# Kernel optimization log

Measured on AMD Instinct MI355X. Metric: run time of the kernel, lower is better.

The kernel has to match this reference:

```python
import jax, jax.numpy as jnp
import numpy as np
import math

D_MODEL = 1024
NUM_HEADS = 16
D_K = D_MODEL // NUM_HEADS
THETA = 10000.0
NEG_INF = 1.0e6  # module uses -1e6, not -inf


def _rope_tables(seq_len):
    pair_idx = jnp.arange(0, D_K, 2, dtype=jnp.float32)
    inv_freq = 1.0 / (THETA ** (pair_idx / D_K))
    pos = jnp.arange(seq_len, dtype=jnp.float32)
    angles = jnp.outer(pos, inv_freq)  # (S, D_K//2)
    return jnp.cos(angles), jnp.sin(angles)


def _apply_rope(x, cos, sin):
    # x: (B, H, S, D_K); cos/sin: (S, D_K//2)
    xe = x[..., 0::2]
    xo = x[..., 1::2]
    oe = xe * cos - xo * sin
    oo = xe * sin + xo * cos
    return jnp.stack([oe, oo], axis=-1).reshape(x.shape)


def setup_inputs() -> dict:
    key = jax.random.key(0)
    k0, k1, k2, k3, k4 = jax.random.split(key, 5)
    B, S = 2, 2048
    x = jax.random.normal(k0, (B, S, D_MODEL), dtype=jnp.float32)
    scale = 0.02
    wq = jax.random.normal(k1, (D_MODEL, D_MODEL), dtype=jnp.float32) * scale
    wk = jax.random.normal(k2, (D_MODEL, D_MODEL), dtype=jnp.float32) * scale
    wv = jax.random.normal(k3, (D_MODEL, D_MODEL), dtype=jnp.float32) * scale
    wo = jax.random.normal(k4, (D_MODEL, D_MODEL), dtype=jnp.float32) * scale
    return {"x": x, "wq": wq, "wk": wk, "wv": wv, "wo": wo}


def reference(x, wq, wk, wv, wo):
    B, S, _ = x.shape
    q = x @ wq.T
    k = x @ wk.T
    v = x @ wv.T
    # (B, S, H, d_k) -> (B, H, S, d_k)
    q = q.reshape(B, S, NUM_HEADS, D_K).transpose(0, 2, 1, 3)
    k = k.reshape(B, S, NUM_HEADS, D_K).transpose(0, 2, 1, 3)
    v = v.reshape(B, S, NUM_HEADS, D_K).transpose(0, 2, 1, 3)
    cos, sin = _rope_tables(S)
    q = _apply_rope(q, cos, sin)
    k = _apply_rope(k, cos, sin)
    scores = jnp.einsum("bhqd,bhkd->bhqk", q, k) / math.sqrt(D_K)
    causal = jnp.tril(jnp.ones((S, S), dtype=bool))
    scores = jnp.where(causal, scores, -NEG_INF)
    attn = jax.nn.softmax(scores, axis=-1)
    out = jnp.einsum("bhqk,bhkd->bhqd", attn, v)
    out = out.transpose(0, 2, 1, 3).reshape(B, S, D_MODEL)
    return out @ wo.T
```

## Files before the change

### kernel.cpp

```cpp
#include <hip/hip_runtime.h>

typedef __attribute__((ext_vector_type(8))) __bf16 bf16x8;
typedef __attribute__((ext_vector_type(8))) _Float16 f16x8;
typedef __attribute__((ext_vector_type(4))) float f32x4;
typedef __attribute__((ext_vector_type(8))) unsigned short u16x8;

#define MFMA_BF16(a, b, c) __builtin_amdgcn_mfma_f32_16x16x32_bf16((a), (b), (c), 0, 0, 0)
#define MFMA_F16(a, b, c)  __builtin_amdgcn_mfma_f32_16x16x32_f16((a), (b), (c), 0, 0, 0)
#define LOG2E 1.44269504088896340736f
#define QSCALE 0.18033688011112042f

__device__ __forceinline__ float b2f(unsigned short u) {
    union { unsigned int i; float f; } v; v.i = ((unsigned int)u) << 16; return v.f;
}
__device__ __forceinline__ unsigned short f2bf(float f) {
    union { float f; unsigned int i; } v; v.f = f;
    unsigned int u = v.i;
    return (unsigned short)((u + 0x7fffu + ((u >> 16) & 1u)) >> 16);
}

__device__ __forceinline__ void gl_lds16(const void* g, void* l) {
    __builtin_amdgcn_global_load_lds(
        (const __attribute__((address_space(1))) void*)g,
        (__attribute__((address_space(3))) void*)l,
        16, 0, 0);
}

__global__ __launch_bounds__(256) void cvt_all(const float* __restrict__ x,
                                               const float* __restrict__ wq,
                                               const float* __restrict__ wk,
                                               const float* __restrict__ wv,
                                               const float* __restrict__ wo,
                                               unsigned short* __restrict__ xb,
                                               unsigned short* __restrict__ wqb,
                                               unsigned short* __restrict__ wkb,
                                               unsigned short* __restrict__ wvb,
                                               unsigned short* __restrict__ wob) {
    int id = blockIdx.x * 256 + threadIdx.x;
    const float* src; unsigned short* dst; size_t off; float scl = 1.0f;
    if (id < 524288)      { src = x;  dst = xb;  off = (size_t)id * 8; }
    else if (id < 655360) { src = wq; dst = wqb; off = (size_t)(id - 524288) * 8; scl = QSCALE; }
    else if (id < 786432) { src = wk; dst = wkb; off = (size_t)(id - 655360) * 8; }
    else if (id < 917504) { src = wv; dst = wvb; off = (size_t)(id - 786432) * 8; }
    else                  { src = wo; dst = wob; off = (size_t)(id - 917504) * 8; }
    float4 a = *(const float4*)(src + off);
    float4 b = *(const float4*)(src + off + 4);
    u16x8 o;
    o[0] = f2bf(a.x * scl); o[1] = f2bf(a.y * scl); o[2] = f2bf(a.z * scl); o[3] = f2bf(a.w * scl);
    o[4] = f2bf(b.x * scl); o[5] = f2bf(b.y * scl); o[6] = f2bf(b.z * scl); o[7] = f2bf(b.w * scl);
    *(u16x8*)(dst + off) = o;
}

template <int MODE>
__device__ __forceinline__ void gemm128_bt(const unsigned short* __restrict__ A,
                                           const unsigned short* __restrict__ B,
                                           void* __restrict__ Cv,
                                           int m0, int n0, int ldc,
                                           unsigned short* As, unsigned short* Bs) {
    const int tid = threadIdx.x;
    const int w = tid >> 6, lane = tid & 63;
    const int quad = lane >> 4, l15 = lane & 15;
    const int wm = w & 1, wn = w >> 1;

    f32x4 acc[4][4];
#pragma unroll
    for (int mt = 0; mt < 4; ++mt)
#pragma unroll
        for (int nt = 0; nt < 4; ++nt) acc[mt][nt] = f32x4{0.f, 0.f, 0.f, 0.f};

    for (int k0 = 0; k0 < 1024; k0 += 32) {
        __syncthreads();
#pragma unroll
        for (int i = 0; i < 2; ++i) {
            int L = (w * 2 + i) * 64 + lane;
            int r = L >> 2;
            int c = (L & 3) ^ ((r >> 1) & 3);
            gl_lds16(A + (size_t)(m0 + r) * 1024 + k0 + c * 8, As + L * 8);
            gl_lds16(B + (size_t)(n0 + r) * 1024 + k0 + c * 8, Bs + L * 8);
        }
        __syncthreads();

        bf16x8 af[4], bfr[4];
#pragma unroll
        for (int mt = 0; mt < 4; ++mt) {
            int row = wm * 64 + mt * 16 + l15;
            af[mt] = *(const bf16x8*)(As + row * 32 + (quad ^ ((row >> 1) & 3)) * 8);
        }
#pragma unroll
        for (int nt = 0; nt < 4; ++nt) {
            int row = wn * 64 + nt * 16 + l15;
            bfr[nt] = *(const bf16x8*)(Bs + row * 32 + (quad ^ ((row >> 1) & 3)) * 8);
        }
#pragma unroll
        for (int mt = 0; mt < 4; ++mt)
#pragma unroll
            for (int nt = 0; nt < 4; ++nt)
                acc[mt][nt] = MFMA_BF16(af[mt], bfr[nt], acc[mt][nt]);
    }

    float invf[4], sgn = 0.f;
    if constexpr (MODE == 3) {
        sgn = (l15 & 1) ? 1.0f : -1.0f;
#pragma unroll
        for (int nt = 0; nt < 4; ++nt)
            invf[nt] = exp2f(-0.41524101186092029f * (float)((nt * 16 + l15) >> 1));
    }

#pragma unroll
    for (int mt = 0; mt < 4; ++mt) {
        int grow = m0 + wm * 64 + mt * 16 + quad * 4;
#pragma unroll
        for (int nt = 0; nt < 4; ++nt) {
            int gcol = n0 + wn * 64 + nt * 16 + l15;
#pragma unroll
            for (int r = 0; r < 4; ++r) {
                float val = acc[mt][nt][r];
                size_t idx = (size_t)(grow + r) * ldc + gcol;
                if constexpr (MODE == 0) {
                    ((unsigned short*)Cv)[idx] = f2bf(val);
                } else if constexpr (MODE == 1) {
                    ((float*)Cv)[idx] = val;
                } else if constexpr (MODE == 2) {
                    _Float16 hv = (_Float16)val;
                    ((unsigned short*)Cv)[idx] = __builtin_bit_cast(unsigned short, hv);
                } else {
                    float p = __shfl_xor(val, 1);
                    float pos = (float)((grow + r) & 2047);
                    float ang = pos * invf[nt];
                    float out = val * __cosf(ang) + sgn * p * __sinf(ang);
                    ((unsigned short*)Cv)[idx] = f2bf(out);
                }
            }
        }
    }
}

__global__ __launch_bounds__(256) void gemm_qkv(const unsigned short* __restrict__ X,
                                                const unsigned short* __restrict__ Wq,
                                                const unsigned short* __restrict__ Wk,
                                                const unsigned short* __restrict__ Wv,
                                                unsigned short* __restrict__ Qo,
                                                unsigned short* __restrict__ Ko,
                                                unsigned short* __restrict__ Vt) {
    __shared__ unsigned short As[128 * 32];
    __shared__ unsigned short Bs[128 * 32];
    int y = blockIdx.y;
    if (y < 16) {
        int sel = y >> 3;
        int m0 = blockIdx.x * 128;
        int n0 = (y & 7) * 128;
        const unsigned short* B = sel ? Wk : Wq;
        unsigned short* C = sel ? Ko : Qo;
        gemm128_bt<3>(X, B, C, m0, n0, 1024, As, Bs);
    } else {
        int m0 = (y & 7) * 128;
        int n0 = blockIdx.x * 128;
        gemm128_bt<2>(Wv, X, Vt, m0, n0, 4096, As, Bs);
    }
}

__global__ __launch_bounds__(256) void gemm_out(const unsigned short* __restrict__ A,
                                                const unsigned short* __restrict__ Wo,
                                                float* __restrict__ C) {
    __shared__ unsigned short As[128 * 32];
    __shared__ unsigned short Bs[128 * 32];
    gemm128_bt<1>(A, Wo, C, blockIdx.x * 128, blockIdx.y * 128, 1024, As, Bs);
}

#define FBODY(KB, MASKED)                                                               \
    {                                                                                   \
        const int kb_ = (KB);                                                           \
        f32x4 sc[4];                                                                    \
        _Pragma("unroll")                                                               \
        for (int nt = 0; nt < 4; ++nt) {                                                \
            int row = nt * 16 + l15;                                                    \
            int cof = (quad ^ (row & 7)) * 8;                                           \
            bf16x8 kf0 = *(const bf16x8*)(Ks + row * 64 + cof);                         \
            bf16x8 kf1 = *(const bf16x8*)(Ks + row * 64 + (cof ^ 32));                  \
            f32x4 z = f32x4{0.f, 0.f, 0.f, 0.f};                                        \
            sc[nt] = MFMA_BF16(qf0, kf0, z);                                            \
            sc[nt] = MFMA_BF16(qf1, kf1, sc[nt]);                                       \
        }                                                                               \
        unsigned short* Pw = Ps[w];                                                     \
        _Pragma("unroll")                                                               \
        for (int nt = 0; nt < 4; ++nt) {                                                \
            float e[4];                                                                 \
            _Pragma("unroll")                                                           \
            for (int r = 0; r < 4; ++r) {                                               \
                float ev = exp2f(sc[nt][r]);                                            \
                if (MASKED) {                                                           \
                    int kpos = kb_ * 64 + nt * 16 + l15;                                \
                    int qpos = qpos0 + quad * 4 + r;                                    \
                    ev = (kpos > qpos) ? 0.f : ev;                                      \
                }                                                                       \
                e[r] = ev;                                                              \
            }                                                                           \
            unsigned pk01 = __builtin_bit_cast(unsigned,                                \
                                __builtin_amdgcn_cvt_pkrtz(e[0], e[1]));                \
            unsigned pk23 = __builtin_bit_cast(unsigned,                                \
                                __builtin_amdgcn_cvt_pkrtz(e[2], e[3]));                \
            int col = nt * 16 + l15;                                                    \
            Pw[(quad * 4 + 0) * 72 + col] = (unsigned short)pk01;                       \
            Pw[(quad * 4 + 1) * 72 + col] = (unsigned short)(pk01 >> 16);               \
            Pw[(quad * 4 + 2) * 72 + col] = (unsigned short)pk23;                       \
            Pw[(quad * 4 + 3) * 72 + col] = (unsigned short)(pk23 >> 16);               \
        }                                                                               \
        __asm__ volatile("s_waitcnt lgkmcnt(0)" ::: "memory");                          \
        f16x8 pf0 = *(const f16x8*)(Pw + l15 * 72 + quad * 8);                          \
        f16x8 pf1 = *(const f16x8*)(Pw + l15 * 72 + 32 + quad * 8);                     \
        lacc = MFMA_F16(pf0, ones, lacc);                                               \
        lacc = MFMA_F16(pf1, ones, lacc);                                               \
        _Pragma("unroll")                                                               \
        for (int nt = 0; nt < 4; ++nt) {                                                \
            int row = nt * 16 + l15;                                                    \
            int cof = (quad ^ (row & 7)) * 8;                                           \
            f16x8 vf0 = *(const f16x8*)(Vs + row * 64 + cof);                           \
            f16x8 vf1 = *(const f16x8*)(Vs + row * 64 + (cof ^ 32));                    \
            accO[nt] = MFMA_F16(pf0, vf0, accO[nt]);                                    \
            accO[nt] = MFMA_F16(pf1, vf1, accO[nt]);                                    \
        }                                                                               \
    }

__global__ __launch_bounds__(256) void flash_attn(const unsigned short* __restrict__ Q,
                                                  const unsigned short* __restrict__ Kb,
                                                  const unsigned short* __restrict__ Vt,
                                                  unsigned short* __restrict__ O) {
    int id = blockIdx.x;
    int xcd = id & 7;
    int sl = id >> 3;
    int rr = sl >> 5;
    int j  = sl & 31;
    int qt;
    if (rr == 0)      qt = j;
    else if (rr == 1) qt = 31 - j;
    else if (rr == 2) qt = (j + 16) & 31;
    else              qt = 31 - ((j + 16) & 31);
    int bh = xcd + 8 * rr;
    int b = bh >> 4, h = bh & 15;
    int tid = threadIdx.x, w = tid >> 6, lane = tid & 63;
    int quad = lane >> 4, l15 = lane & 15;
    int qrow0 = b * 2048 + qt * 64 + w * 16;
    int qpos0 = qt * 64 + w * 16;

    __shared__ unsigned short Ks[64 * 64];
    __shared__ unsigned short Vs[64 * 64];
    __shared__ unsigned short Ps[4][16 * 72];

    bf16x8 qf0, qf1;
    {
        const unsigned short* qp = Q + (size_t)(qrow0 + l15) * 1024 + h * 64 + quad * 8;
        qf0 = *(const bf16x8*)qp;
        qf1 = *(const bf16x8*)(qp + 32);
    }
    f16x8 ones;
#pragma unroll
    for (int jj = 0; jj < 8; ++jj) ones[jj] = (_Float16)1.0f;

    int L0 = w * 128 + lane;
    int L1 = L0 + 64;
    int r0 = L0 >> 3, c0s = (L0 & 7) ^ (r0 & 7);
    int r1 = L1 >> 3, c1s = (L1 & 7) ^ (r1 & 7);
    const unsigned short* Kg0 = Kb + (size_t)(b * 2048 + r0) * 1024 + h * 64 + c0s * 8;
    const unsigned short* Kg1 = Kb + (size_t)(b * 2048 + r1) * 1024 + h * 64 + c1s * 8;
    const unsigned short* Vg0 = Vt + (size_t)(h * 64 + r0) * 4096 + b * 2048 + c0s * 8;
    const unsigned short* Vg1 = Vt + (size_t)(h * 64 + r1) * 4096 + b * 2048 + c1s * 8;

    f32x4 accO[4];
#pragma unroll
    for (int nt = 0; nt < 4; ++nt) accO[nt] = f32x4{0.f, 0.f, 0.f, 0.f};
    f32x4 lacc = f32x4{0.f, 0.f, 0.f, 0.f};

    for (int kb = 0; kb <= qt; ++kb) {
        __syncthreads();
        {
            size_t ko = (size_t)kb * 64 * 1024;
            size_t vo = (size_t)kb * 64;
            gl_lds16(Kg0 + ko, Ks + L0 * 8);
            gl_lds16(Kg1 + ko, Ks + L1 * 8);
            gl_lds16(Vg0 + vo, Vs + L0 * 8);
            gl_lds16(Vg1 + vo, Vs + L1 * 8);
        }
        __syncthreads();
        if (kb < qt) {
            FBODY(kb, 0)
        } else {
            FBODY(kb, 1)
        }
    }

    float inv[4];
#pragma unroll
    for (int r = 0; r < 4; ++r) inv[r] = 1.0f / lacc[r];
#pragma unroll
    for (int nt = 0; nt < 4; ++nt)
#pragma unroll
        for (int r = 0; r < 4; ++r)
            O[(size_t)(qrow0 + quad * 4 + r) * 1024 + h * 64 + nt * 16 + l15] =
                f2bf(accO[nt][r] * inv[r]);
}

extern "C" void kernel_launch(void* const* d_in, const int* in_sizes, int n_in,
                              void* d_out, int out_size, void* d_ws, size_t ws_size,
                              hipStream_t stream) {
    (void)in_sizes; (void)n_in; (void)out_size; (void)ws_size;
    const float* x  = (const float*)d_in[0];
    const float* wq = (const float*)d_in[1];
    const float* wk = (const float*)d_in[2];
    const float* wv = (const float*)d_in[3];
    const float* wo = (const float*)d_in[4];
    float* out = (float*)d_out;

    const size_t T = (size_t)4096 * 1024;
    const size_t W = (size_t)1024 * 1024;
    unsigned short* Q   = (unsigned short*)d_ws;
    unsigned short* K   = Q + T;
    unsigned short* Vt  = K + T;
    unsigned short* xb  = Vt + T;
    unsigned short* AO  = xb;
    unsigned short* wqb = xb + T;
    unsigned short* wkb = wqb + W;
    unsigned short* wvb = wkb + W;
    unsigned short* wob = wvb + W;

    cvt_all  <<<dim3(4096),   256, 0, stream>>>(x, wq, wk, wv, wo, xb, wqb, wkb, wvb, wob);
    gemm_qkv <<<dim3(32, 24), 256, 0, stream>>>(xb, wqb, wkb, wvb, Q, K, Vt);
    flash_attn<<<dim3(1024),  256, 0, stream>>>(Q, K, Vt, AO);
    gemm_out <<<dim3(32, 8),  256, 0, stream>>>(AO, wob, out);
}
```

Before: 187.3 us.

## Switch flash attention to 32x32 MFMA tiles with two waves per block

Rewrites the flash attention inner loop to use 32x32x16 MFMA instructions. Each wave now owns 32 query rows instead of 16, and the block shrinks from four waves to two, with a launch bound of 128 threads and 3 blocks per CU. The aim is fewer MFMA issues and fewer LDS reads per unit of work, since K/V fragments are reused across 32 query rows. In exchange, per-wave register pressure rises (16-wide accumulators), P writes to LDS become scalar per element, and there are fewer waves per block to hide load latency.

```diff
diff --git a/kernel.cpp b/kernel.cpp
--- a/kernel.cpp
+++ b/kernel.cpp
@@ -3,10 +3,12 @@
 typedef __attribute__((ext_vector_type(8))) __bf16 bf16x8;
 typedef __attribute__((ext_vector_type(8))) _Float16 f16x8;
 typedef __attribute__((ext_vector_type(4))) float f32x4;
+typedef __attribute__((ext_vector_type(16))) float f32x16;
 typedef __attribute__((ext_vector_type(8))) unsigned short u16x8;
 
 #define MFMA_BF16(a, b, c) __builtin_amdgcn_mfma_f32_16x16x32_bf16((a), (b), (c), 0, 0, 0)
-#define MFMA_F16(a, b, c)  __builtin_amdgcn_mfma_f32_16x16x32_f16((a), (b), (c), 0, 0, 0)
+#define MFMA32_BF16(a, b, c) __builtin_amdgcn_mfma_f32_32x32x16_bf16((a), (b), (c), 0, 0, 0)
+#define MFMA32_F16(a, b, c)  __builtin_amdgcn_mfma_f32_32x32x16_f16((a), (b), (c), 0, 0, 0)
 #define LOG2E 1.44269504088896340736f
 #define QSCALE 0.18033688011112042f
 
@@ -167,64 +169,53 @@
     gemm128_bt<1>(A, Wo, C, blockIdx.x * 128, blockIdx.y * 128, 1024, As, Bs);
 }
 
-#define FBODY(KB, MASKED)                                                               \
+#define FBODY32(KB, MASKED)                                                             \
     {                                                                                   \
         const int kb_ = (KB);                                                           \
-        f32x4 sc[4];                                                                    \
-        _Pragma("unroll")                                                               \
-        for (int nt = 0; nt < 4; ++nt) {                                                \
-            int row = nt * 16 + l15;                                                    \
-            int cof = (quad ^ (row & 7)) * 8;                                           \
-            bf16x8 kf0 = *(const bf16x8*)(Ks + row * 64 + cof);                         \
-            bf16x8 kf1 = *(const bf16x8*)(Ks + row * 64 + (cof ^ 32));                  \
-            f32x4 z = f32x4{0.f, 0.f, 0.f, 0.f};                                        \
-            sc[nt] = MFMA_BF16(qf0, kf0, z);                                            \
-            sc[nt] = MFMA_BF16(qf1, kf1, sc[nt]);                                       \
+        f32x16 s0 = {0.f}, s1 = {0.f};                                                  \
+        _Pragma("unroll")                                                               \
+        for (int kc = 0; kc < 4; ++kc) {                                                \
+            int ch = kc * 2 + hi;                                                       \
+            bf16x8 kf0 = *(const bf16x8*)(Ks + k31 * 64 + ((ch ^ (k31 & 7)) * 8));      \
+            bf16x8 kf1 = *(const bf16x8*)(Ks + (32 + k31) * 64 + ((ch ^ (k31 & 7)) * 8));\
+            s0 = MFMA32_BF16(qf[kc], kf0, s0);                                          \
+            s1 = MFMA32_BF16(qf[kc], kf1, s1);                                          \
         }                                                                               \
-        unsigned short* Pw = Ps[w];                                                     \
-        _Pragma("unroll")                                                               \
-        for (int nt = 0; nt < 4; ++nt) {                                                \
-            float e[4];                                                                 \
-            _Pragma("unroll")                                                           \
-            for (int r = 0; r < 4; ++r) {                                               \
-                float ev = exp2f(sc[nt][r]);                                            \
-                if (MASKED) {                                                           \
-                    int kpos = kb_ * 64 + nt * 16 + l15;                                \
-                    int qpos = qpos0 + quad * 4 + r;                                    \
-                    ev = (kpos > qpos) ? 0.f : ev;                                      \
-                }                                                                       \
-                e[r] = ev;                                                              \
+        _Pragma("unroll")                                                               \
+        for (int r = 0; r < 16; ++r) {                                                  \
+            int qrow = (r & 3) + 8 * (r >> 2) + 4 * hi;                                 \
+            float e0 = exp2f(s0[r]);                                                    \
+            float e1 = exp2f(s1[r]);                                                    \
+            if (MASKED) {                                                               \
+                int qpos = qpos0 + qrow;                                                \
+                e0 = (kb_ * 64 + k31 > qpos) ? 0.f : e0;                                \
+                e1 = (kb_ * 64 + 32 + k31 > qpos) ? 0.f : e1;                           \
             }                                                                           \
-            unsigned pk01 = __builtin_bit_cast(unsigned,                                \
-                                __builtin_amdgcn_cvt_pkrtz(e[0], e[1]));                \
-            unsigned pk23 = __builtin_bit_cast(unsigned,                                \
-                                __builtin_amdgcn_cvt_pkrtz(e[2], e[3]));                \
-            int col = nt * 16 + l15;                                                    \
-            Pw[(quad * 4 + 0) * 72 + col] = (unsigned short)pk01;                       \
-            Pw[(quad * 4 + 1) * 72 + col] = (unsigned short)(pk01 >> 16);               \
-            Pw[(quad * 4 + 2) * 72 + col] = (unsigned short)pk23;                       \
-            Pw[(quad * 4 + 3) * 72 + col] = (unsigned short)(pk23 >> 16);               \
+            _Float16 h0 = (_Float16)e0, h1 = (_Float16)e1;                              \
+            Pw[qrow * 72 + k31]      = __builtin_bit_cast(unsigned short, h0);          \
+            Pw[qrow * 72 + 32 + k31] = __builtin_bit_cast(unsigned short, h1);          \
         }                                                                               \
         __asm__ volatile("s_waitcnt lgkmcnt(0)" ::: "memory");                          \
-        f16x8 pf0 = *(const f16x8*)(Pw + l15 * 72 + quad * 8);                          \
-        f16x8 pf1 = *(const f16x8*)(Pw + l15 * 72 + 32 + quad * 8);                     \
-        lacc = MFMA_F16(pf0, ones, lacc);                                               \
-        lacc = MFMA_F16(pf1, ones, lacc);                                               \
-        _Pragma("unroll")                                                               \
-        for (int nt = 0; nt < 4; ++nt) {                                                \
-            int row = nt * 16 + l15;                                                    \
-            int cof = (quad ^ (row & 7)) * 8;                                           \
-            f16x8 vf0 = *(const f16x8*)(Vs + row * 64 + cof);                           \
-            f16x8 vf1 = *(const f16x8*)(Vs + row * 64 + (cof ^ 32));                    \
-            accO[nt] = MFMA_F16(pf0, vf0, accO[nt]);                                    \
-            accO[nt] = MFMA_F16(pf1, vf1, accO[nt]);                                    \
+        f16x8 pf[4];                                                                    \
+        _Pragma("unroll")                                                               \
+        for (int kc = 0; kc < 4; ++kc)                                                  \
+            pf[kc] = *(const f16x8*)(Pw + k31 * 72 + kc * 16 + hi * 8);                 \
+        _Pragma("unroll")                                                               \
+        for (int kc = 0; kc < 4; ++kc) lacc = MFMA32_F16(pf[kc], ones, lacc);           \
+        _Pragma("unroll")                                                               \
+        for (int kc = 0; kc < 4; ++kc) {                                                \
+            int ch = kc * 2 + hi;                                                       \
+            f16x8 vf0 = *(const f16x8*)(Vs + k31 * 64 + ((ch ^ (k31 & 7)) * 8));        \
+            f16x8 vf1 = *(const f16x8*)(Vs + (32 + k31) * 64 + ((ch ^ (k31 & 7)) * 8)); \
+            accO0 = MFMA32_F16(pf[kc], vf0, accO0);                                     \
+            accO1 = MFMA32_F16(pf[kc], vf1, accO1);                                     \
         }                                                                               \
     }
 
-__global__ __launch_bounds__(256) void flash_attn(const unsigned short* __restrict__ Q,
-                                                  const unsigned short* __restrict__ Kb,
-                                                  const unsigned short* __restrict__ Vt,
-                                                  unsigned short* __restrict__ O) {
+__global__ __launch_bounds__(128, 3) void flash_attn(const unsigned short* __restrict__ Q,
+                                                     const unsigned short* __restrict__ Kb,
+                                                     const unsigned short* __restrict__ Vt,
+                                                     unsigned short* __restrict__ O) {
     int id = blockIdx.x;
     int xcd = id & 7;
     int sl = id >> 3;
@@ -238,65 +229,69 @@
     int bh = xcd + 8 * rr;
     int b = bh >> 4, h = bh & 15;
     int tid = threadIdx.x, w = tid >> 6, lane = tid & 63;
-    int quad = lane >> 4, l15 = lane & 15;
-    int qrow0 = b * 2048 + qt * 64 + w * 16;
-    int qpos0 = qt * 64 + w * 16;
+    const int k31 = lane & 31, hi = lane >> 5;
+    int qbase = b * 2048 + qt * 64 + w * 32;
+    int qpos0 = qt * 64 + w * 32;
 
     __shared__ unsigned short Ks[64 * 64];
     __shared__ unsigned short Vs[64 * 64];
-    __shared__ unsigned short Ps[4][16 * 72];
-
-    bf16x8 qf0, qf1;
-    {
-        const unsigned short* qp = Q + (size_t)(qrow0 + l15) * 1024 + h * 64 + quad * 8;
-        qf0 = *(const bf16x8*)qp;
-        qf1 = *(const bf16x8*)(qp + 32);
-    }
+    __shared__ unsigned short Ps[2][32 * 72];
+
+    bf16x8 qf[4];
+#pragma unroll
+    for (int kc = 0; kc < 4; ++kc)
+        qf[kc] = *(const bf16x8*)(Q + (size_t)(qbase + k31) * 1024 + h * 64 + kc * 16 + hi * 8);
+
     f16x8 ones;
 #pragma unroll
     for (int jj = 0; jj < 8; ++jj) ones[jj] = (_Float16)1.0f;
 
-    int L0 = w * 128 + lane;
-    int L1 = L0 + 64;
-    int r0 = L0 >> 3, c0s = (L0 & 7) ^ (r0 & 7);
-    int r1 = L1 >> 3, c1s = (L1 & 7) ^ (r1 & 7);
-    const unsigned short* Kg0 = Kb + (size_t)(b * 2048 + r0) * 1024 + h * 64 + c0s * 8;
-    const unsigned short* Kg1 = Kb + (size_t)(b * 2048 + r1) * 1024 + h * 64 + c1s * 8;
-    const unsigned short* Vg0 = Vt + (size_t)(h * 64 + r0) * 4096 + b * 2048 + c0s * 8;
-    const unsigned short* Vg1 = Vt + (size_t)(h * 64 + r1) * 4096 + b * 2048 + c1s * 8;
-
-    f32x4 accO[4];
-#pragma unroll
-    for (int nt = 0; nt < 4; ++nt) accO[nt] = f32x4{0.f, 0.f, 0.f, 0.f};
-    f32x4 lacc = f32x4{0.f, 0.f, 0.f, 0.f};
+    const unsigned short* KgA[4];
+    const unsigned short* VgA[4];
+    int Ldst[4];
+#pragma unroll
+    for (int i = 0; i < 4; ++i) {
+        int L = i * 128 + tid;
+        int r = L >> 3, cpos = L & 7;
+        int c = cpos ^ (r & 7);
+        Ldst[i] = L * 8;
+        KgA[i] = Kb + (size_t)(b * 2048 + r) * 1024 + h * 64 + c * 8;
+        VgA[i] = Vt + (size_t)(h * 64 + r) * 4096 + b * 2048 + c * 8;
+    }
+
+    f32x16 accO0 = {0.f}, accO1 = {0.f};
+    f32x16 lacc = {0.f};
+    unsigned short* Pw = Ps[w];
 
     for (int kb = 0; kb <= qt; ++kb) {
         __syncthreads();
         {
             size_t ko = (size_t)kb * 64 * 1024;
             size_t vo = (size_t)kb * 64;
-            gl_lds16(Kg0 + ko, Ks + L0 * 8);
-            gl_lds16(Kg1 + ko, Ks + L1 * 8);
-            gl_lds16(Vg0 + vo, Vs + L0 * 8);
-            gl_lds16(Vg1 + vo, Vs + L1 * 8);
+#pragma unroll
+            for (int i = 0; i < 4; ++i) {
+                gl_lds16(KgA[i] + ko, Ks + Ldst[i]);
+                gl_lds16(VgA[i] + vo, Vs + Ldst[i]);
+            }
         }
         __syncthreads();
         if (kb < qt) {
-            FBODY(kb, 0)
+            FBODY32(kb, 0)
         } else {
-            FBODY(kb, 1)
-        }
-    }
-
-    float inv[4];
-#pragma unroll
-    for (int r = 0; r < 4; ++r) inv[r] = 1.0f / lacc[r];
-#pragma unroll
-    for (int nt = 0; nt < 4; ++nt)
-#pragma unroll
-        for (int r = 0; r < 4; ++r)
-            O[(size_t)(qrow0 + quad * 4 + r) * 1024 + h * 64 + nt * 16 + l15] =
-                f2bf(accO[nt][r] * inv[r]);
+            FBODY32(kb, 1)
+        }
+    }
+
+    float inv[16];
+#pragma unroll
+    for (int r = 0; r < 16; ++r) inv[r] = 1.0f / lacc[r];
+#pragma unroll
+    for (int r = 0; r < 16; ++r) {
+        int qrow = (r & 3) + 8 * (r >> 2) + 4 * hi;
+        size_t base = (size_t)(qbase + qrow) * 1024 + h * 64;
+        O[base + k31]      = f2bf(accO0[r] * inv[r]);
+        O[base + 32 + k31] = f2bf(accO1[r] * inv[r]);
+    }
 }
 
 extern "C" void kernel_launch(void* const* d_in, const int* in_sizes, int n_in,
@@ -324,6 +319,6 @@
 
     cvt_all  <<<dim3(4096),   256, 0, stream>>>(x, wq, wk, wv, wo, xb, wqb, wkb, wvb, wob);
     gemm_qkv <<<dim3(32, 24), 256, 0, stream>>>(xb, wqb, wkb, wvb, Q, K, Vt);
-    flash_attn<<<dim3(1024),  256, 0, stream>>>(Q, K, Vt, AO);
+    flash_attn<<<dim3(1024),  128, 0, stream>>>(Q, K, Vt, AO);
     gemm_out <<<dim3(32, 8),  256, 0, stream>>>(AO, wob, out);
 }
```

After: 247.8 us. 32.3% more time.

## Process two 64-row query tiles per attention block to reuse K/V tiles

Applied to the files above, without the earlier changes.

Each flash-attention workgroup now handles 128 query rows, as two 64-row sub-tiles per wave, instead of 64. Every K/V tile loaded into LDS therefore feeds twice as many MFMAs, which halves global-to-LDS traffic and barrier count per unit of work. The grid shrinks from 1024 to 512 blocks and the block-to-tile mapping changes. The last two diagonal key blocks are peeled with specialised masking and skipping. In exchange, register pressure roughly doubles for accumulators, there are fewer blocks to hide latency, and causal load balance gets coarser.

```diff
diff --git a/kernel.cpp b/kernel.cpp
--- a/kernel.cpp
+++ b/kernel.cpp
@@ -167,10 +167,10 @@
     gemm128_bt<1>(A, Wo, C, blockIdx.x * 128, blockIdx.y * 128, 1024, As, Bs);
 }
 
-#define FBODY(KB, MASKED)                                                               \
+#define FB(KB, M0, M1)                                                                  \
     {                                                                                   \
         const int kb_ = (KB);                                                           \
-        f32x4 sc[4];                                                                    \
+        f32x4 s0[4], s1[4];                                                             \
         _Pragma("unroll")                                                               \
         for (int nt = 0; nt < 4; ++nt) {                                                \
             int row = nt * 16 + l15;                                                    \
@@ -178,79 +178,108 @@
             bf16x8 kf0 = *(const bf16x8*)(Ks + row * 64 + cof);                         \
             bf16x8 kf1 = *(const bf16x8*)(Ks + row * 64 + (cof ^ 32));                  \
             f32x4 z = f32x4{0.f, 0.f, 0.f, 0.f};                                        \
-            sc[nt] = MFMA_BF16(qf0, kf0, z);                                            \
-            sc[nt] = MFMA_BF16(qf1, kf1, sc[nt]);                                       \
+            if (M0 != 2) {                                                              \
+                s0[nt] = MFMA_BF16(qf[0][0], kf0, z);                                   \
+                s0[nt] = MFMA_BF16(qf[0][1], kf1, s0[nt]);                              \
+            }                                                                           \
+            s1[nt] = MFMA_BF16(qf[1][0], kf0, z);                                       \
+            s1[nt] = MFMA_BF16(qf[1][1], kf1, s1[nt]);                                  \
         }                                                                               \
-        unsigned short* Pw = Ps[w];                                                     \
         _Pragma("unroll")                                                               \
-        for (int nt = 0; nt < 4; ++nt) {                                                \
-            float e[4];                                                                 \
+        for (int t = 0; t < 2; ++t) {                                                   \
+            if (t == 0 && M0 == 2) continue;                                            \
+            f32x4* sp = t ? s1 : s0;                                                    \
+            const int msk = t ? M1 : M0;                                                \
+            unsigned short* Pw = Ps[w][t];                                              \
             _Pragma("unroll")                                                           \
-            for (int r = 0; r < 4; ++r) {                                               \
-                float ev = exp2f(sc[nt][r]);                                            \
-                if (MASKED) {                                                           \
-                    int kpos = kb_ * 64 + nt * 16 + l15;                                \
-                    int qpos = qpos0 + quad * 4 + r;                                    \
-                    ev = (kpos > qpos) ? 0.f : ev;                                      \
+            for (int nt = 0; nt < 4; ++nt) {                                            \
+                float e[4];                                                             \
+                _Pragma("unroll")                                                       \
+                for (int r = 0; r < 4; ++r) {                                           \
+                    float ev = exp2f(sp[nt][r]);                                        \
+                    if (msk == 1) {                                                     \
+                        int kpos = kb_ * 64 + nt * 16 + l15;                            \
+                        int qpos = qpos0 + t * 64 + quad * 4 + r;                       \
+                        ev = (kpos > qpos) ? 0.f : ev;                                  \
+                    }                                                                   \
+                    e[r] = ev;                                                          \
                 }                                                                       \
-                e[r] = ev;                                                              \
+                unsigned pk01 = __builtin_bit_cast(unsigned,                            \
+                                    __builtin_amdgcn_cvt_pkrtz(e[0], e[1]));            \
+                unsigned pk23 = __builtin_bit_cast(unsigned,                            \
+                                    __builtin_amdgcn_cvt_pkrtz(e[2], e[3]));            \
+                int col = nt * 16 + l15;                                                \
+                Pw[(quad * 4 + 0) * 72 + col] = (unsigned short)pk01;                   \
+                Pw[(quad * 4 + 1) * 72 + col] = (unsigned short)(pk01 >> 16);           \
+                Pw[(quad * 4 + 2) * 72 + col] = (unsigned short)pk23;                   \
+                Pw[(quad * 4 + 3) * 72 + col] = (unsigned short)(pk23 >> 16);           \
             }                                                                           \
-            unsigned pk01 = __builtin_bit_cast(unsigned,                                \
-                                __builtin_amdgcn_cvt_pkrtz(e[0], e[1]));                \
-            unsigned pk23 = __builtin_bit_cast(unsigned,                                \
-                                __builtin_amdgcn_cvt_pkrtz(e[2], e[3]));                \
-            int col = nt * 16 + l15;                                                    \
-            Pw[(quad * 4 + 0) * 72 + col] = (unsigned short)pk01;                       \
-            Pw[(quad * 4 + 1) * 72 + col] = (unsigned short)(pk01 >> 16);               \
-            Pw[(quad * 4 + 2) * 72 + col] = (unsigned short)pk23;                       \
-            Pw[(quad * 4 + 3) * 72 + col] = (unsigned short)(pk23 >> 16);               \
         }                                                                               \
         __asm__ volatile("s_waitcnt lgkmcnt(0)" ::: "memory");                          \
-        f16x8 pf0 = *(const f16x8*)(Pw + l15 * 72 + quad * 8);                          \
-        f16x8 pf1 = *(const f16x8*)(Pw + l15 * 72 + 32 + quad * 8);                     \
-        lacc = MFMA_F16(pf0, ones, lacc);                                               \
-        lacc = MFMA_F16(pf1, ones, lacc);                                               \
+        f16x8 pf0a, pf1a, pf0b, pf1b;                                                   \
+        if (M0 != 2) {                                                                  \
+            pf0a = *(const f16x8*)(Ps[w][0] + l15 * 72 + quad * 8);                     \
+            pf1a = *(const f16x8*)(Ps[w][0] + l15 * 72 + 32 + quad * 8);                \
+            lacc[0] = MFMA_F16(pf0a, ones, lacc[0]);                                    \
+            lacc[0] = MFMA_F16(pf1a, ones, lacc[0]);                                    \
+        }                                                                               \
+        pf0b = *(const f16x8*)(Ps[w][1] + l15 * 72 + quad * 8);                         \
+        pf1b = *(const f16x8*)(Ps[w][1] + l15 * 72 + 32 + quad * 8);                    \
+        lacc[1] = MFMA_F16(pf0b, ones, lacc[1]);                                        \
+        lacc[1] = MFMA_F16(pf1b, ones, lacc[1]);                                        \
         _Pragma("unroll")                                                               \
         for (int nt = 0; nt < 4; ++nt) {                                                \
             int row = nt * 16 + l15;                                                    \
             int cof = (quad ^ (row & 7)) * 8;                                           \
             f16x8 vf0 = *(const f16x8*)(Vs + row * 64 + cof);                           \
             f16x8 vf1 = *(const f16x8*)(Vs + row * 64 + (cof ^ 32));                    \
-            accO[nt] = MFMA_F16(pf0, vf0, accO[nt]);                                    \
-            accO[nt] = MFMA_F16(pf1, vf1, accO[nt]);                                    \
+            if (M0 != 2) {                                                              \
+                accO[0][nt] = MFMA_F16(pf0a, vf0, accO[0][nt]);                         \
+                accO[0][nt] = MFMA_F16(pf1a, vf1, accO[0][nt]);                         \
+            }                                                                           \
+            accO[1][nt] = MFMA_F16(pf0b, vf0, accO[1][nt]);                             \
+            accO[1][nt] = MFMA_F16(pf1b, vf1, accO[1][nt]);                             \
         }                                                                               \
     }
 
-__global__ __launch_bounds__(256) void flash_attn(const unsigned short* __restrict__ Q,
-                                                  const unsigned short* __restrict__ Kb,
-                                                  const unsigned short* __restrict__ Vt,
-                                                  unsigned short* __restrict__ O) {
+#define STAGE(KB)                                                                       \
+    {                                                                                   \
+        size_t ko = (size_t)(KB) * 64 * 1024;                                           \
+        size_t vo = (size_t)(KB) * 64;                                                  \
+        gl_lds16(Kg0 + ko, Ks + L0 * 8);                                                \
+        gl_lds16(Kg1 + ko, Ks + L1 * 8);                                                \
+        gl_lds16(Vg0 + vo, Vs + L0 * 8);                                                \
+        gl_lds16(Vg1 + vo, Vs + L1 * 8);                                                \
+    }
+
+__global__ __launch_bounds__(256, 4) void flash_attn(const unsigned short* __restrict__ Q,
+                                                     const unsigned short* __restrict__ Kb,
+                                                     const unsigned short* __restrict__ Vt,
+                                                     unsigned short* __restrict__ O) {
     int id = blockIdx.x;
     int xcd = id & 7;
     int sl = id >> 3;
-    int rr = sl >> 5;
-    int j  = sl & 31;
-    int qt;
-    if (rr == 0)      qt = j;
-    else if (rr == 1) qt = 31 - j;
-    else if (rr == 2) qt = (j + 16) & 31;
-    else              qt = 31 - ((j + 16) & 31);
+    int rr = sl >> 4;
+    int j  = sl & 15;
+    int qt = (rr & 1) ? (15 - j) : j;
     int bh = xcd + 8 * rr;
     int b = bh >> 4, h = bh & 15;
     int tid = threadIdx.x, w = tid >> 6, lane = tid & 63;
     int quad = lane >> 4, l15 = lane & 15;
-    int qrow0 = b * 2048 + qt * 64 + w * 16;
-    int qpos0 = qt * 64 + w * 16;
+    int qbase = b * 2048 + qt * 128 + w * 16;
+    int qpos0 = qt * 128 + w * 16;
 
     __shared__ unsigned short Ks[64 * 64];
     __shared__ unsigned short Vs[64 * 64];
-    __shared__ unsigned short Ps[4][16 * 72];
-
-    bf16x8 qf0, qf1;
-    {
-        const unsigned short* qp = Q + (size_t)(qrow0 + l15) * 1024 + h * 64 + quad * 8;
-        qf0 = *(const bf16x8*)qp;
-        qf1 = *(const bf16x8*)(qp + 32);
+    __shared__ unsigned short Ps[4][2][16 * 72];
+
+    bf16x8 qf[2][2];
+#pragma unroll
+    for (int t = 0; t < 2; ++t) {
+        const unsigned short* qp =
+            Q + (size_t)(qbase + t * 64 + l15) * 1024 + h * 64 + quad * 8;
+        qf[t][0] = *(const bf16x8*)qp;
+        qf[t][1] = *(const bf16x8*)(qp + 32);
     }
     f16x8 ones;
 #pragma unroll
@@ -265,38 +294,41 @@
     const unsigned short* Vg0 = Vt + (size_t)(h * 64 + r0) * 4096 + b * 2048 + c0s * 8;
     const unsigned short* Vg1 = Vt + (size_t)(h * 64 + r1) * 4096 + b * 2048 + c1s * 8;
 
-    f32x4 accO[4];
-#pragma unroll
-    for (int nt = 0; nt < 4; ++nt) accO[nt] = f32x4{0.f, 0.f, 0.f, 0.f};
-    f32x4 lacc = f32x4{0.f, 0.f, 0.f, 0.f};
-
-    for (int kb = 0; kb <= qt; ++kb) {
+    f32x4 accO[2][4];
+#pragma unroll
+    for (int t = 0; t < 2; ++t)
+#pragma unroll
+        for (int nt = 0; nt < 4; ++nt) accO[t][nt] = f32x4{0.f, 0.f, 0.f, 0.f};
+    f32x4 lacc[2] = {f32x4{0.f, 0.f, 0.f, 0.f}, f32x4{0.f, 0.f, 0.f, 0.f}};
+
+    int nkb2 = 2 * qt;
+    for (int kb = 0; kb < nkb2; ++kb) {
         __syncthreads();
-        {
-            size_t ko = (size_t)kb * 64 * 1024;
-            size_t vo = (size_t)kb * 64;
-            gl_lds16(Kg0 + ko, Ks + L0 * 8);
-            gl_lds16(Kg1 + ko, Ks + L1 * 8);
-            gl_lds16(Vg0 + vo, Vs + L0 * 8);
-            gl_lds16(Vg1 + vo, Vs + L1 * 8);
-        }
+        STAGE(kb)
         __syncthreads();
-        if (kb < qt) {
-            FBODY(kb, 0)
-        } else {
-            FBODY(kb, 1)
-        }
-    }
-
-    float inv[4];
-#pragma unroll
-    for (int r = 0; r < 4; ++r) inv[r] = 1.0f / lacc[r];
-#pragma unroll
-    for (int nt = 0; nt < 4; ++nt)
-#pragma unroll
-        for (int r = 0; r < 4; ++r)
-            O[(size_t)(qrow0 + quad * 4 + r) * 1024 + h * 64 + nt * 16 + l15] =
-                f2bf(accO[nt][r] * inv[r]);
+        FB(kb, 0, 0)
+    }
+    __syncthreads();
+    STAGE(nkb2)
+    __syncthreads();
+    FB(nkb2, 1, 0)
+    __syncthreads();
+    STAGE(nkb2 + 1)
+    __syncthreads();
+    FB(nkb2 + 1, 2, 1)
+
+#pragma unroll
+    for (int t = 0; t < 2; ++t) {
+        float inv[4];
+#pragma unroll
+        for (int r = 0; r < 4; ++r) inv[r] = 1.0f / lacc[t][r];
+#pragma unroll
+        for (int nt = 0; nt < 4; ++nt)
+#pragma unroll
+            for (int r = 0; r < 4; ++r)
+                O[(size_t)(qbase + t * 64 + quad * 4 + r) * 1024 + h * 64 + nt * 16 + l15] =
+                    f2bf(accO[t][nt][r] * inv[r]);
+    }
 }
 
 extern "C" void kernel_launch(void* const* d_in, const int* in_sizes, int n_in,
@@ -324,6 +356,6 @@
 
     cvt_all  <<<dim3(4096),   256, 0, stream>>>(x, wq, wk, wv, wo, xb, wqb, wkb, wvb, wob);
     gemm_qkv <<<dim3(32, 24), 256, 0, stream>>>(xb, wqb, wkb, wvb, Q, K, Vt);
-    flash_attn<<<dim3(1024),  256, 0, stream>>>(Q, K, Vt, AO);
+    flash_attn<<<dim3(512),   256, 0, stream>>>(Q, K, Vt, AO);
     gemm_out <<<dim3(32, 8),  256, 0, stream>>>(AO, wob, out);
 }
```

Measured after the change: 200.2 us. +6.9%, slower.
